# Kernel optimization log

Hardware: AMD Instinct MI355X
Metric: run time of the kernel (lower is better)

## Reference

```python
import jax, jax.numpy as jnp
import numpy as np

B, N, C, H = 2, 2048, 768, 12
HD = C // H  # head dim = 64


def setup_inputs() -> dict:
    key = jax.random.key(0)
    k1, k2, k3 = jax.random.split(key, 3)
    x = jax.random.normal(k1, (B, N, C), dtype=jnp.float32)
    w_qkv = jax.random.normal(k2, (C, 3 * C), dtype=jnp.float32) * (C ** -0.5)
    w_proj = jax.random.normal(k3, (C, C), dtype=jnp.float32) * (C ** -0.5)
    b_proj = jnp.zeros((C,), dtype=jnp.float32)
    return {"x": x, "w_qkv": w_qkv, "w_proj": w_proj, "b_proj": b_proj}


def reference(x, w_qkv, w_proj, b_proj):
    scale = HD ** -0.5
    # qkv projection: [B,N,3C] -> [3,B,H,N,HD]
    qkv = (x @ w_qkv).reshape(B, N, 3, H, HD).transpose(2, 0, 3, 1, 4)
    q, k, v = qkv[0], qkv[1], qkv[2]
    # explicit QK^T softmax V (materializes [B,H,N,N] scores, as in source)
    attn = jnp.einsum("bhqd,bhkd->bhqk", q, k) * scale
    attn = jax.nn.softmax(attn, axis=-1)
    out = jnp.einsum("bhqk,bhkd->bhqd", attn, v)
    out = out.transpose(0, 2, 1, 3).reshape(B, N, C)
    return out @ w_proj + b_proj
```

## Files before the change

kernel.cpp:

```cpp
#include <hip/hip_runtime.h>

#define C_DIM 768
#define NSEQ 2048
#define H_DIM 12
#define HD 64
#define M_ROWS 4096

typedef float f32x4 __attribute__((ext_vector_type(4)));
typedef short bf16x8 __attribute__((ext_vector_type(8)));
typedef unsigned short u16;

__device__ __forceinline__ u16 f2bf(float f) {
  union { float f; unsigned u; } v; v.f = f;
  unsigned u = v.u + 0x7FFFu + ((v.u >> 16) & 1u);
  return (u16)(u >> 16);
}

__global__ __launch_bounds__(256) void cvt_x_kernel(const float* __restrict__ in,
                                                    u16* __restrict__ out, int n4) {
  int i = blockIdx.x * 256 + threadIdx.x;
  if (i < n4) {
    float4 v = ((const float4*)in)[i];
    ushort4 o;
    o.x = f2bf(v.x); o.y = f2bf(v.y); o.z = f2bf(v.z); o.w = f2bf(v.w);
    ((ushort4*)out)[i] = o;
  }
}

__global__ __launch_bounds__(256) void transpose_cvt_kernel(const float* __restrict__ in,
                                                            u16* __restrict__ out,
                                                            int R, int Cc) {
  __shared__ float t[32][33];
  int tx = threadIdx.x & 31, ty = threadIdx.x >> 5;
  int c0 = blockIdx.x * 32, r0 = blockIdx.y * 32;
#pragma unroll
  for (int i = 0; i < 4; i++)
    t[ty + i * 8][tx] = in[(size_t)(r0 + ty + i * 8) * Cc + c0 + tx];
  __syncthreads();
#pragma unroll
  for (int i = 0; i < 4; i++)
    out[(size_t)(c0 + ty + i * 8) * R + r0 + tx] = f2bf(t[tx][ty + i * 8]);
}

__device__ __forceinline__ void gemm_core_128(const u16* __restrict__ A,
                                              const u16* __restrict__ BT,
                                              int m0, int n0,
                                              u16* la, u16* lb, f32x4 acc[4][4]) {
  const int K = C_DIM;
  int tid = threadIdx.x;
  int lane = tid & 63, wave = tid >> 6;
  int wm = (wave >> 1) * 64, wn = (wave & 1) * 64;
  int quad = lane >> 4, l16 = lane & 15;

  int rowA = tid >> 2, cj = tid & 3;
  const u16* pa0 = A + (size_t)(m0 + rowA) * K + cj * 8;
  const u16* pa1 = pa0 + (size_t)64 * K;
  const u16* pb0 = BT + (size_t)(n0 + rowA) * K + cj * 8;
  const u16* pb1 = pb0 + (size_t)64 * K;
  int swz = ((cj ^ (rowA & 3)) * 8);
  int wr0 = rowA * 32 + swz;
  int wr1 = (rowA + 64) * 32 + swz;

  for (int k0 = 0; k0 < K; k0 += 32) {
    uint4 va0 = *(const uint4*)(pa0 + k0);
    uint4 va1 = *(const uint4*)(pa1 + k0);
    uint4 vb0 = *(const uint4*)(pb0 + k0);
    uint4 vb1 = *(const uint4*)(pb1 + k0);
    __syncthreads();
    *(uint4*)(la + wr0) = va0;
    *(uint4*)(la + wr1) = va1;
    *(uint4*)(lb + wr0) = vb0;
    *(uint4*)(lb + wr1) = vb1;
    __syncthreads();
    bf16x8 af[4], bfr[4];
#pragma unroll
    for (int mt = 0; mt < 4; mt++) {
      int r = wm + mt * 16 + l16;
      af[mt] = *(const bf16x8*)(la + r * 32 + ((quad ^ (r & 3)) * 8));
    }
#pragma unroll
    for (int nt = 0; nt < 4; nt++) {
      int r = wn + nt * 16 + l16;
      bfr[nt] = *(const bf16x8*)(lb + r * 32 + ((quad ^ (r & 3)) * 8));
    }
#pragma unroll
    for (int mt = 0; mt < 4; mt++)
#pragma unroll
      for (int nt = 0; nt < 4; nt++)
        acc[mt][nt] = __builtin_amdgcn_mfma_f32_16x16x32_bf16(af[mt], bfr[nt], acc[mt][nt], 0, 0, 0);
  }
}

#define Q_PRESCALE 0.18033688011112042f
__global__ __launch_bounds__(256) void gemm_qkv_kernel(const u16* __restrict__ A,
                                                       const u16* __restrict__ BT,
                                                       u16* __restrict__ qb,
                                                       u16* __restrict__ kb,
                                                       u16* __restrict__ vtb) {
  __shared__ __align__(16) u16 la[128 * 32];
  __shared__ __align__(16) u16 lb[128 * 32];
  f32x4 acc[4][4] = {};
  int m0 = blockIdx.x * 128, n0 = blockIdx.y * 128;
  gemm_core_128(A, BT, m0, n0, la, lb, acc);

  int lane = threadIdx.x & 63, wave = threadIdx.x >> 6;
  int wm = (wave >> 1) * 64, wn = (wave & 1) * 64;
  int quad = lane >> 4, l16 = lane & 15;
#pragma unroll
  for (int mt = 0; mt < 4; mt++) {
#pragma unroll
    for (int nt = 0; nt < 4; nt++) {
      int gn = n0 + wn + nt * 16 + l16;
      int which = gn / C_DIM;
      int cc = gn - which * C_DIM;
      int h = cc >> 6, d = cc & 63;
#pragma unroll
      for (int r = 0; r < 4; r++) {
        int gm = m0 + wm + mt * 16 + quad * 4 + r;
        int b = gm >> 11, n = gm & 2047;
        float val = acc[mt][nt][r];
        size_t bh = (size_t)(b * H_DIM + h);
        if (which == 0)
          qb[(bh * NSEQ + n) * HD + d] = f2bf(val * Q_PRESCALE);
        else if (which == 1)
          kb[(bh * NSEQ + n) * HD + d] = f2bf(val);
        else
          vtb[(bh * HD + d) * NSEQ + n] = f2bf(val);
      }
    }
  }
}

__global__ __launch_bounds__(256) void gemm_proj_kernel(const u16* __restrict__ A,
                                                        const u16* __restrict__ BT,
                                                        const float* __restrict__ bias,
                                                        float* __restrict__ out) {
  __shared__ __align__(16) u16 la[128 * 32];
  __shared__ __align__(16) u16 lb[128 * 32];
  f32x4 acc[4][4] = {};
  int m0 = blockIdx.x * 128, n0 = blockIdx.y * 128;
  gemm_core_128(A, BT, m0, n0, la, lb, acc);

  int lane = threadIdx.x & 63, wave = threadIdx.x >> 6;
  int wm = (wave >> 1) * 64, wn = (wave & 1) * 64;
  int quad = lane >> 4, l16 = lane & 15;
#pragma unroll
  for (int mt = 0; mt < 4; mt++) {
#pragma unroll
    for (int nt = 0; nt < 4; nt++) {
      int gn = n0 + wn + nt * 16 + l16;
      float bv = bias[gn];
#pragma unroll
      for (int r = 0; r < 4; r++) {
        int gm = m0 + wm + mt * 16 + quad * 4 + r;
        out[(size_t)gm * C_DIM + gn] = acc[mt][nt][r] + bv;
      }
    }
  }
}

__global__ __launch_bounds__(256) void attn_kernel(const u16* __restrict__ qb,
                                                   const u16* __restrict__ kb,
                                                   const u16* __restrict__ vtb,
                                                   u16* __restrict__ attn) {
  __shared__ __align__(16) u16 lk[2][64 * 72];
  __shared__ __align__(16) u16 lv[2][64 * 72];
  __shared__ __align__(16) u16 lp[4][16 * 72];
  int bh = blockIdx.y, qt = blockIdx.x;
  int tid = threadIdx.x, lane = tid & 63, wave = tid >> 6;
  int quad = lane >> 4, l16 = lane & 15;

  const u16* q_bh = qb + (size_t)bh * NSEQ * HD;
  const u16* k_bh = kb + (size_t)bh * NSEQ * HD;
  const u16* v_bh = vtb + (size_t)bh * HD * NSEQ;

  size_t qrow = (size_t)(qt * 64 + wave * 16 + l16) * HD;
  bf16x8 qf0 = *(const bf16x8*)(q_bh + qrow + quad * 8);
  bf16x8 qf1 = *(const bf16x8*)(q_bh + qrow + 32 + quad * 8);

  f32x4 o[4] = {};
  float l_i[4] = {0.f, 0.f, 0.f, 0.f};

  int srow = tid >> 3, scj = tid & 7;
  const u16* kp0 = k_bh + (size_t)srow * HD + scj * 8;
  const u16* kp1 = kp0 + (size_t)32 * HD;
  const u16* vp0 = v_bh + (size_t)srow * NSEQ + scj * 8;
  const u16* vp1 = vp0 + (size_t)32 * NSEQ;
  int w0 = srow * 72 + scj * 8, w1 = (srow + 32) * 72 + scj * 8;

  {
    uint4 rk0 = *(const uint4*)(kp0);
    uint4 rk1 = *(const uint4*)(kp1);
    uint4 rv0 = *(const uint4*)(vp0);
    uint4 rv1 = *(const uint4*)(vp1);
    *(uint4*)(lk[0] + w0) = rk0;
    *(uint4*)(lk[0] + w1) = rk1;
    *(uint4*)(lv[0] + w0) = rv0;
    *(uint4*)(lv[0] + w1) = rv1;
  }

  u16* lpw = lp[wave];

  for (int kt = 0; kt < 32; kt++) {
    int cur = kt & 1, nxt = cur ^ 1;
    __syncthreads();

    uint4 rk0, rk1, rv0, rv1;
    if (kt < 31) {
      int k0 = (kt + 1) * 64;
      rk0 = *(const uint4*)(kp0 + (size_t)k0 * HD);
      rk1 = *(const uint4*)(kp1 + (size_t)k0 * HD);
      rv0 = *(const uint4*)(vp0 + k0);
      rv1 = *(const uint4*)(vp1 + k0);
    }

    f32x4 s[4] = {};
#pragma unroll
    for (int nt = 0; nt < 4; nt++) {
      const u16* bp = lk[cur] + (nt * 16 + l16) * 72;
      bf16x8 b0 = *(const bf16x8*)(bp + quad * 8);
      bf16x8 b1 = *(const bf16x8*)(bp + 32 + quad * 8);
      s[nt] = __builtin_amdgcn_mfma_f32_16x16x32_bf16(qf0, b0, s[nt], 0, 0, 0);
      s[nt] = __builtin_amdgcn_mfma_f32_16x16x32_bf16(qf1, b1, s[nt], 0, 0, 0);
    }

#pragma unroll
    for (int nt = 0; nt < 4; nt++) {
#pragma unroll
      for (int r = 0; r < 4; r++) {
        float p = __builtin_amdgcn_exp2f(s[nt][r]);
        l_i[r] += p;
        lpw[(quad * 4 + r) * 72 + nt * 16 + l16] = f2bf(p);
      }
    }

#pragma unroll
    for (int ks = 0; ks < 2; ks++) {
      bf16x8 pf = *(const bf16x8*)(lpw + l16 * 72 + ks * 32 + quad * 8);
#pragma unroll
      for (int dt = 0; dt < 4; dt++) {
        bf16x8 vf = *(const bf16x8*)(lv[cur] + (dt * 16 + l16) * 72 + ks * 32 + quad * 8);
        o[dt] = __builtin_amdgcn_mfma_f32_16x16x32_bf16(pf, vf, o[dt], 0, 0, 0);
      }
    }

    if (kt < 31) {
      *(uint4*)(lk[nxt] + w0) = rk0;
      *(uint4*)(lk[nxt] + w1) = rk1;
      *(uint4*)(lv[nxt] + w0) = rv0;
      *(uint4*)(lv[nxt] + w1) = rv1;
    }
  }

#pragma unroll
  for (int r = 0; r < 4; r++) {
#pragma unroll
    for (int off = 1; off < 16; off <<= 1) l_i[r] += __shfl_xor(l_i[r], off);
  }

  int b = bh / H_DIM, h = bh % H_DIM;
#pragma unroll
  for (int r = 0; r < 4; r++) {
    float inv = 1.f / l_i[r];
    int gq = b * NSEQ + qt * 64 + wave * 16 + quad * 4 + r;
#pragma unroll
    for (int dt = 0; dt < 4; dt++)
      attn[(size_t)gq * C_DIM + h * HD + dt * 16 + l16] = f2bf(o[dt][r] * inv);
  }
}

extern "C" void kernel_launch(void* const* d_in, const int* in_sizes, int n_in,
                              void* d_out, int out_size, void* d_ws, size_t ws_size,
                              hipStream_t stream) {
  const float* x = (const float*)d_in[0];
  const float* w_qkv = (const float*)d_in[1];
  const float* w_proj = (const float*)d_in[2];
  const float* b_proj = (const float*)d_in[3];
  float* out = (float*)d_out;

  char* ws = (char*)d_ws;
  u16* x_bf   = (u16*)(ws);
  u16* wqkvT  = (u16*)(ws + 6291456);
  u16* wprojT = (u16*)(ws + 9830400);
  u16* qb     = (u16*)(ws + 11010048);
  u16* kb     = (u16*)(ws + 17301504);
  u16* vtb    = (u16*)(ws + 23592960);
  u16* attn   = x_bf;

  cvt_x_kernel<<<3072, 256, 0, stream>>>(x, x_bf, M_ROWS * C_DIM / 4);
  transpose_cvt_kernel<<<dim3(72, 24), 256, 0, stream>>>(w_qkv, wqkvT, C_DIM, 3 * C_DIM);
  transpose_cvt_kernel<<<dim3(24, 24), 256, 0, stream>>>(w_proj, wprojT, C_DIM, C_DIM);
  gemm_qkv_kernel<<<dim3(32, 18), 256, 0, stream>>>(x_bf, wqkvT, qb, kb, vtb);
  attn_kernel<<<dim3(32, 24), 256, 0, stream>>>(qb, kb, vtb, attn);
  gemm_proj_kernel<<<dim3(32, 6), 256, 0, stream>>>(attn, wprojT, b_proj, out);
}
```

Before: 188.9 us.

## Use fp16 Q/K/V, register-resident P via transposed MFMA, 128-query attention tiles

Q, K and V^T are now stored as fp16 rather than bf16. The attention kernel computes S^T = K·Q^T, so the exp'd probabilities land directly in the B-operand layout of a 16x16x16 f16 MFMA. This removes the per-wave LDS round trip for P. Each block now handles 128 queries (two 16-row tiles per wave), so every K/V tile loaded into LDS is reused twice as much and the grid is halved. The V^T store in the QKV GEMM becomes a vectorized 4-wide write. The risks are fp16 overflow of unnormalized exp values (still no max subtraction), more register pressure, and fewer blocks.

```diff
diff --git a/kernel.cpp b/kernel.cpp
--- a/kernel.cpp
+++ b/kernel.cpp
@@ -8,7 +8,12 @@
 
 typedef float f32x4 __attribute__((ext_vector_type(4)));
 typedef short bf16x8 __attribute__((ext_vector_type(8)));
+typedef _Float16 f16x8 __attribute__((ext_vector_type(8)));
+typedef _Float16 f16x4 __attribute__((ext_vector_type(4)));
+typedef __fp16 fp16x2 __attribute__((ext_vector_type(2)));
 typedef unsigned short u16;
+
+#define MFMA_PV(a, b, c) __builtin_amdgcn_mfma_f32_16x16x16f16(a, b, c, 0, 0, 0)
 
 __device__ __forceinline__ u16 f2bf(float f) {
   union { float f; unsigned u; } v; v.f = f;
@@ -94,9 +99,9 @@
 #define Q_PRESCALE 0.18033688011112042f
 __global__ __launch_bounds__(256) void gemm_qkv_kernel(const u16* __restrict__ A,
                                                        const u16* __restrict__ BT,
-                                                       u16* __restrict__ qb,
-                                                       u16* __restrict__ kb,
-                                                       u16* __restrict__ vtb) {
+                                                       _Float16* __restrict__ qb,
+                                                       _Float16* __restrict__ kb,
+                                                       _Float16* __restrict__ vtb) {
   __shared__ __align__(16) u16 la[128 * 32];
   __shared__ __align__(16) u16 lb[128 * 32];
   f32x4 acc[4][4] = {};
@@ -114,18 +119,22 @@
       int which = gn / C_DIM;
       int cc = gn - which * C_DIM;
       int h = cc >> 6, d = cc & 63;
-#pragma unroll
-      for (int r = 0; r < 4; r++) {
-        int gm = m0 + wm + mt * 16 + quad * 4 + r;
-        int b = gm >> 11, n = gm & 2047;
-        float val = acc[mt][nt][r];
-        size_t bh = (size_t)(b * H_DIM + h);
-        if (which == 0)
-          qb[(bh * NSEQ + n) * HD + d] = f2bf(val * Q_PRESCALE);
-        else if (which == 1)
-          kb[(bh * NSEQ + n) * HD + d] = f2bf(val);
-        else
-          vtb[(bh * HD + d) * NSEQ + n] = f2bf(val);
+      int gm0 = m0 + wm + mt * 16 + quad * 4;
+      int b = gm0 >> 11, n = gm0 & 2047;
+      size_t bh = (size_t)(b * H_DIM + h);
+      if (which == 2) {
+        f16x4 hv;
+#pragma unroll
+        for (int r = 0; r < 4; r++) hv[r] = (_Float16)acc[mt][nt][r];
+        *(f16x4*)(vtb + (bh * HD + d) * NSEQ + n) = hv;
+      } else if (which == 0) {
+#pragma unroll
+        for (int r = 0; r < 4; r++)
+          qb[(bh * NSEQ + n + r) * HD + d] = (_Float16)(acc[mt][nt][r] * Q_PRESCALE);
+      } else {
+#pragma unroll
+        for (int r = 0; r < 4; r++)
+          kb[(bh * NSEQ + n + r) * HD + d] = (_Float16)acc[mt][nt][r];
       }
     }
   }
@@ -159,27 +168,31 @@
   }
 }
 
-__global__ __launch_bounds__(256) void attn_kernel(const u16* __restrict__ qb,
-                                                   const u16* __restrict__ kb,
-                                                   const u16* __restrict__ vtb,
+__global__ __launch_bounds__(256) void attn_kernel(const _Float16* __restrict__ qb,
+                                                   const _Float16* __restrict__ kb,
+                                                   const _Float16* __restrict__ vtb,
                                                    u16* __restrict__ attn) {
   __shared__ __align__(16) u16 lk[2][64 * 72];
   __shared__ __align__(16) u16 lv[2][64 * 72];
-  __shared__ __align__(16) u16 lp[4][16 * 72];
-  int bh = blockIdx.y, qt = blockIdx.x;
+  int bh = blockIdx.y, qblk = blockIdx.x;
   int tid = threadIdx.x, lane = tid & 63, wave = tid >> 6;
   int quad = lane >> 4, l16 = lane & 15;
 
-  const u16* q_bh = qb + (size_t)bh * NSEQ * HD;
-  const u16* k_bh = kb + (size_t)bh * NSEQ * HD;
-  const u16* v_bh = vtb + (size_t)bh * HD * NSEQ;
-
-  size_t qrow = (size_t)(qt * 64 + wave * 16 + l16) * HD;
-  bf16x8 qf0 = *(const bf16x8*)(q_bh + qrow + quad * 8);
-  bf16x8 qf1 = *(const bf16x8*)(q_bh + qrow + 32 + quad * 8);
-
-  f32x4 o[4] = {};
-  float l_i[4] = {0.f, 0.f, 0.f, 0.f};
+  const _Float16* q_bh = qb + (size_t)bh * NSEQ * HD;
+  const u16* k_bh = (const u16*)(kb + (size_t)bh * NSEQ * HD);
+  const u16* v_bh = (const u16*)(vtb + (size_t)bh * HD * NSEQ);
+
+  int q0 = qblk * 128 + wave * 32 + l16;
+  f16x8 qf[2][2];
+#pragma unroll
+  for (int qt = 0; qt < 2; qt++) {
+    const _Float16* qp = q_bh + (size_t)(q0 + qt * 16) * HD + quad * 8;
+    qf[qt][0] = *(const f16x8*)qp;
+    qf[qt][1] = *(const f16x8*)(qp + 32);
+  }
+
+  f32x4 o[2][4] = {};
+  float l_i[2] = {0.f, 0.f};
 
   int srow = tid >> 3, scj = tid & 7;
   const u16* kp0 = k_bh + (size_t)srow * HD + scj * 8;
@@ -189,17 +202,11 @@
   int w0 = srow * 72 + scj * 8, w1 = (srow + 32) * 72 + scj * 8;
 
   {
-    uint4 rk0 = *(const uint4*)(kp0);
-    uint4 rk1 = *(const uint4*)(kp1);
-    uint4 rv0 = *(const uint4*)(vp0);
-    uint4 rv1 = *(const uint4*)(vp1);
-    *(uint4*)(lk[0] + w0) = rk0;
-    *(uint4*)(lk[0] + w1) = rk1;
-    *(uint4*)(lv[0] + w0) = rv0;
-    *(uint4*)(lv[0] + w1) = rv1;
-  }
-
-  u16* lpw = lp[wave];
+    *(uint4*)(lk[0] + w0) = *(const uint4*)(kp0);
+    *(uint4*)(lk[0] + w1) = *(const uint4*)(kp1);
+    *(uint4*)(lv[0] + w0) = *(const uint4*)(vp0);
+    *(uint4*)(lv[0] + w1) = *(const uint4*)(vp1);
+  }
 
   for (int kt = 0; kt < 32; kt++) {
     int cur = kt & 1, nxt = cur ^ 1;
@@ -214,33 +221,42 @@
       rv1 = *(const uint4*)(vp1 + k0);
     }
 
-    f32x4 s[4] = {};
-#pragma unroll
-    for (int nt = 0; nt < 4; nt++) {
-      const u16* bp = lk[cur] + (nt * 16 + l16) * 72;
-      bf16x8 b0 = *(const bf16x8*)(bp + quad * 8);
-      bf16x8 b1 = *(const bf16x8*)(bp + 32 + quad * 8);
-      s[nt] = __builtin_amdgcn_mfma_f32_16x16x32_bf16(qf0, b0, s[nt], 0, 0, 0);
-      s[nt] = __builtin_amdgcn_mfma_f32_16x16x32_bf16(qf1, b1, s[nt], 0, 0, 0);
-    }
-
-#pragma unroll
-    for (int nt = 0; nt < 4; nt++) {
-#pragma unroll
-      for (int r = 0; r < 4; r++) {
-        float p = __builtin_amdgcn_exp2f(s[nt][r]);
-        l_i[r] += p;
-        lpw[(quad * 4 + r) * 72 + nt * 16 + l16] = f2bf(p);
-      }
-    }
-
-#pragma unroll
-    for (int ks = 0; ks < 2; ks++) {
-      bf16x8 pf = *(const bf16x8*)(lpw + l16 * 72 + ks * 32 + quad * 8);
+    f32x4 s0[4], s1[4];
+#pragma unroll
+    for (int nt = 0; nt < 4; nt++) {
+      const u16* kp = lk[cur] + (nt * 16 + l16) * 72 + quad * 8;
+      f16x8 kf0 = *(const f16x8*)kp;
+      f16x8 kf1 = *(const f16x8*)(kp + 32);
+      f32x4 t0 = {}, t1 = {};
+      t0 = __builtin_amdgcn_mfma_f32_16x16x32_f16(kf0, qf[0][0], t0, 0, 0, 0);
+      t0 = __builtin_amdgcn_mfma_f32_16x16x32_f16(kf1, qf[0][1], t0, 0, 0, 0);
+      t1 = __builtin_amdgcn_mfma_f32_16x16x32_f16(kf0, qf[1][0], t1, 0, 0, 0);
+      t1 = __builtin_amdgcn_mfma_f32_16x16x32_f16(kf1, qf[1][1], t1, 0, 0, 0);
+      s0[nt] = t0; s1[nt] = t1;
+    }
+
+#pragma unroll
+    for (int nt = 0; nt < 4; nt++) {
+      float a0 = __builtin_amdgcn_exp2f(s0[nt][0]);
+      float a1 = __builtin_amdgcn_exp2f(s0[nt][1]);
+      float a2 = __builtin_amdgcn_exp2f(s0[nt][2]);
+      float a3 = __builtin_amdgcn_exp2f(s0[nt][3]);
+      l_i[0] += (a0 + a1) + (a2 + a3);
+      float b0 = __builtin_amdgcn_exp2f(s1[nt][0]);
+      float b1 = __builtin_amdgcn_exp2f(s1[nt][1]);
+      float b2 = __builtin_amdgcn_exp2f(s1[nt][2]);
+      float b3 = __builtin_amdgcn_exp2f(s1[nt][3]);
+      l_i[1] += (b0 + b1) + (b2 + b3);
+      union { fp16x2 h2[2]; f16x4 h4; } pa, pb;
+      pa.h2[0] = __builtin_amdgcn_cvt_pkrtz(a0, a1);
+      pa.h2[1] = __builtin_amdgcn_cvt_pkrtz(a2, a3);
+      pb.h2[0] = __builtin_amdgcn_cvt_pkrtz(b0, b1);
+      pb.h2[1] = __builtin_amdgcn_cvt_pkrtz(b2, b3);
 #pragma unroll
       for (int dt = 0; dt < 4; dt++) {
-        bf16x8 vf = *(const bf16x8*)(lv[cur] + (dt * 16 + l16) * 72 + ks * 32 + quad * 8);
-        o[dt] = __builtin_amdgcn_mfma_f32_16x16x32_bf16(pf, vf, o[dt], 0, 0, 0);
+        f16x4 vf = *(const f16x4*)(lv[cur] + (dt * 16 + l16) * 72 + nt * 16 + quad * 4);
+        o[0][dt] = MFMA_PV(vf, pa.h4, o[0][dt]);
+        o[1][dt] = MFMA_PV(vf, pb.h4, o[1][dt]);
       }
     }
 
@@ -253,19 +269,26 @@
   }
 
 #pragma unroll
-  for (int r = 0; r < 4; r++) {
-#pragma unroll
-    for (int off = 1; off < 16; off <<= 1) l_i[r] += __shfl_xor(l_i[r], off);
+  for (int qt = 0; qt < 2; qt++) {
+    l_i[qt] += __shfl_xor(l_i[qt], 16);
+    l_i[qt] += __shfl_xor(l_i[qt], 32);
   }
 
   int b = bh / H_DIM, h = bh % H_DIM;
 #pragma unroll
-  for (int r = 0; r < 4; r++) {
-    float inv = 1.f / l_i[r];
-    int gq = b * NSEQ + qt * 64 + wave * 16 + quad * 4 + r;
-#pragma unroll
-    for (int dt = 0; dt < 4; dt++)
-      attn[(size_t)gq * C_DIM + h * HD + dt * 16 + l16] = f2bf(o[dt][r] * inv);
+  for (int qt = 0; qt < 2; qt++) {
+    float inv = 1.f / l_i[qt];
+    int q = q0 + qt * 16;
+    u16* orow = attn + (size_t)(b * NSEQ + q) * C_DIM + h * HD;
+#pragma unroll
+    for (int dt = 0; dt < 4; dt++) {
+      ushort4 ov;
+      ov.x = f2bf(o[qt][dt][0] * inv);
+      ov.y = f2bf(o[qt][dt][1] * inv);
+      ov.z = f2bf(o[qt][dt][2] * inv);
+      ov.w = f2bf(o[qt][dt][3] * inv);
+      *(ushort4*)(orow + dt * 16 + quad * 4) = ov;
+    }
   }
 }
 
@@ -279,18 +302,18 @@
   float* out = (float*)d_out;
 
   char* ws = (char*)d_ws;
-  u16* x_bf   = (u16*)(ws);
-  u16* wqkvT  = (u16*)(ws + 6291456);
-  u16* wprojT = (u16*)(ws + 9830400);
-  u16* qb     = (u16*)(ws + 11010048);
-  u16* kb     = (u16*)(ws + 17301504);
-  u16* vtb    = (u16*)(ws + 23592960);
-  u16* attn   = x_bf;
+  u16* x_bf        = (u16*)(ws);
+  u16* wqkvT       = (u16*)(ws + 6291456);
+  u16* wprojT      = (u16*)(ws + 9830400);
+  _Float16* qb     = (_Float16*)(ws + 11010048);
+  _Float16* kb     = (_Float16*)(ws + 17301504);
+  _Float16* vtb    = (_Float16*)(ws + 23592960);
+  u16* attn        = x_bf;
 
   cvt_x_kernel<<<3072, 256, 0, stream>>>(x, x_bf, M_ROWS * C_DIM / 4);
   transpose_cvt_kernel<<<dim3(72, 24), 256, 0, stream>>>(w_qkv, wqkvT, C_DIM, 3 * C_DIM);
   transpose_cvt_kernel<<<dim3(24, 24), 256, 0, stream>>>(w_proj, wprojT, C_DIM, C_DIM);
   gemm_qkv_kernel<<<dim3(32, 18), 256, 0, stream>>>(x_bf, wqkvT, qb, kb, vtb);
-  attn_kernel<<<dim3(32, 24), 256, 0, stream>>>(qb, kb, vtb, attn);
+  attn_kernel<<<dim3(16, 24), 256, 0, stream>>>(qb, kb, vtb, attn);
   gemm_proj_kernel<<<dim3(32, 6), 256, 0, stream>>>(attn, wprojT, b_proj, out);
 }
```

Result: faster. 180.1 us (-4.6%).
